# Kernel optimization log

Measured on AMD Instinct MI355X. Metric: run time of the kernel, lower is better.

Reference implementation:

```python
import jax, jax.numpy as jnp
import numpy as np
from jax import lax

# ---- config (mirrors init_kwargs) ----
B, CIN, T, WIDTH = 32, 8, 256, 128
COUT = 64
K = (5, 5)
PAD = (2, 2)            # ceil((k-1)*dilation/2) per dim
OUT_W = 128             # output_shape
EPS = 1e-8
BETA0 = 0.9             # beta 'constant' init, one_per_layer
B0 = 1.0                # b 'constant' init
SIGMA0 = 10.0
MAX_SPK = 3.0           # Max_spikes_per_run


@jax.custom_vjp
def spike_fn(mthr, sigma):
    # Surrogate Heaviside: hard threshold fwd, sigmoid-derivative surrogate bwd.
    return (mthr > 0).astype(mthr.dtype)

def _spike_fwd(mthr, sigma):
    return spike_fn(mthr, sigma), (mthr, sigma)

def _spike_bwd(res, g):
    mthr, sigma = res
    sg = jax.nn.sigmoid(sigma * mthr)
    return (g * sigma * sg * (1.0 - sg), jnp.zeros_like(sigma))

spike_fn.defvjp(_spike_fwd, _spike_bwd)


def setup_inputs() -> dict:
    key = jax.random.key(0)
    kx, kw = jax.random.split(key)
    x = jax.random.normal(kx, (B, CIN, T, WIDTH), dtype=jnp.float32)
    w_std = 1.0 * np.sqrt(1.0 / (CIN * K[0] * K[1]))
    w = jax.random.normal(kw, (COUT, CIN, K[0], K[1]), dtype=jnp.float32) * w_std
    b = jnp.full((COUT,), B0, dtype=jnp.float32)          # clamped >= 0
    beta = jnp.array([BETA0], dtype=jnp.float32)           # one_per_layer, clamped to [0,1]
    sigma = jnp.array([SIGMA0], dtype=jnp.float32)         # surrogate_sigma_mode 'one'
    return {"x": x, "w": w, "b": b, "beta": beta, "sigma": sigma}


def _forward(x, w, b, beta, sigma):
    # conv over (time, width) with 'same'-style padding, then truncate width
    conv_x = lax.conv_general_dilated(
        x, w, window_strides=(1, 1),
        padding=((PAD[0], PAD[0]), (PAD[1], PAD[1])),
        rhs_dilation=(1, 1),
        dimension_numbers=("NCHW", "OIHW", "NCHW"))
    conv_x = conv_x[:, :, :, :OUT_W]                      # [B, COUT, T, OUT_W]

    d = jnp.einsum("oikl,eikl->oe", w, w)                 # lateral matrix [COUT, COUT]
    norm = jnp.sum(w * w, axis=(1, 2, 3))                 # [COUT]
    inv_norm = 1.0 / (norm + EPS)
    beta_s = beta[0]

    conv_seq = jnp.transpose(conv_x, (2, 0, 1, 3))        # [T, B, COUT, OUT_W]

    def step(carry, inp_t):
        mem, spk, prev = carry
        rst = jnp.einsum("bcw,cd->bdw", spk, d)           # lateral reset
        # Leaky neuron, soft reset
        mem = (mem - rst) * beta_s + inp_t * (1.0 - beta_s)
        mthr = mem * inv_norm[None, :, None] - b[None, :, None]
        s = (MAX_SPK - prev) * spike_fn(mthr, sigma)      # spike_limit=True
        prev = prev + s
        return (mem, s, prev), s

    zeros = jnp.zeros((B, COUT, OUT_W), dtype=x.dtype)
    (_, _, _), spk_rec = lax.scan(step, (zeros, zeros, zeros), conv_seq)
    # spk_rec: [T, B, COUT, OUT_W]

    loss = 0.5 * jnp.mean(spk_rec ** 2)                   # 'squared'
    spk_spread = jnp.max(jnp.sum(spk_rec, axis=(1, 2, 3))) / (B * COUT * OUT_W)  # 'max'

    output = jnp.transpose(spk_rec, (1, 2, 0, 3))         # [B, COUT, T, OUT_W]
    return output, loss, spk_spread


def reference(x, w, b, beta, sigma):
    return _forward(x, w, b, beta, sigma)
```

## Files before the change

kernel.cpp:

```cpp
#include <hip/hip_runtime.h>
#include <cstdint>


#define NB 32
#define NC 8
#define NT 256
#define NW 128
#define NO 64
#define WT 16
#define TC 8
#define NROWS 12
#define NCHUNK (NT / TC)
#define XCOLS 20
#define XTILE (NC * NROWS * XCOLS)

__global__ __launch_bounds__(1024)
void prep_kernel(const float* __restrict__ w, float* __restrict__ d3,
                 float* __restrict__ invn, unsigned int* __restrict__ gfires)
{
    __shared__ float wsh[NO * 200];
    const int tid = threadIdx.x;
    for (int i = tid; i < NO * 200; i += 1024) wsh[i] = w[i];
    if (tid < NT) gfires[tid] = 0u;
    __syncthreads();
#pragma unroll
    for (int p = 0; p < 4; ++p) {
        int idx = p * 1024 + tid;
        int o = idx >> 6, e = idx & 63;
        float acc = 0.0f;
        for (int i = 0; i < 200; i += 4) {
            float4 av = *(const float4*)&wsh[o * 200 + i];
            float4 bv = *(const float4*)&wsh[e * 200 + i];
            acc += av.x * bv.x + av.y * bv.y + av.z * bv.z + av.w * bv.w;
        }
        d3[idx] = 3.0f * acc;
        if (o == e) invn[o] = 1.0f / (acc + 1e-8f);
    }
}

__global__ __launch_bounds__(512, 2)
void spk_kernel(const float* __restrict__ x, const float* __restrict__ wglob,
                const float* __restrict__ bias, const float* __restrict__ beta_p,
                const float* __restrict__ d3g, const float* __restrict__ invng,
                float* __restrict__ out, unsigned int* __restrict__ gfires)
{
    __shared__ float wsm[NC * 25 * NO];
    __shared__ float d3s[NO * NO];
    __shared__ float xsh[2][NC][NROWS][XCOLS];
    __shared__ unsigned short tf[2][NO][8];
    __shared__ unsigned int sf[NT];

    const int tid  = threadIdx.x;
    const int lane = tid & 63;
    const int wv   = tid >> 6;
    const int bb   = blockIdx.x >> 3;
    const int w0   = (blockIdx.x & 7) * WT;

    for (int i = tid; i < NC * 25 * NO; i += 512) {
        int co = i & 63; int r = i >> 6;
        int kw = r % 5; int r2 = r / 5; int kt = r2 % 5; int c = r2 / 5;
        wsm[i] = wglob[((co * NC + c) * 5 + kt) * 5 + kw];
    }
    for (int i = tid; i < NO * NO; i += 512) d3s[i] = d3g[i];
    for (int i = tid; i < NT; i += 512) sf[i] = 0u;

    const size_t xbbase = (size_t)bb * NC * NT * NW;
#pragma unroll
    for (int k = 0; k < 4; ++k) {
        int i = tid + k * 512;
        if (i < XTILE) {
            int c = i / (NROWS * XCOLS); int rem = i - c * (NROWS * XCOLS);
            int row = rem / XCOLS; int col = rem - row * XCOLS;
            int tg = row - 2, wg = w0 + col - 2;
            float v = 0.0f;
            if (tg >= 0 && tg < NT && wg >= 0 && wg < NW)
                v = x[xbbase + ((size_t)c * NT + tg) * NW + wg];
            (&xsh[0][0][0][0])[i] = v;
        }
    }

    const float invn = invng[lane];
    const float bco  = bias[lane];
    const float beta = beta_p[0];
    const float omb  = 1.0f - beta;

    float mem0 = 0.f, mem1 = 0.f;
    unsigned int fired = 0u;
    unsigned long long pm0 = 0ull, pm1 = 0ull;

    const int sq = tid & 3;
    const int srow = tid >> 2;

    __syncthreads();

#pragma unroll 1
    for (int ch = 0; ch < NCHUNK; ++ch) {
        const int buf = ch & 1;
        const int tbase = ch * TC;

        float sr0 = 0.f, sr1 = 0.f, sr2 = 0.f, sr3 = 0.f;
        if (ch + 1 < NCHUNK) {
#pragma unroll
            for (int k = 0; k < 4; ++k) {
                int i = tid + k * 512;
                float v = 0.0f;
                if (i < XTILE) {
                    int c = i / (NROWS * XCOLS); int rem = i - c * (NROWS * XCOLS);
                    int row = rem / XCOLS; int col = rem - row * XCOLS;
                    int tg = tbase + 6 + row, wg = w0 + col - 2;
                    if (tg < NT && wg >= 0 && wg < NW)
                        v = x[xbbase + ((size_t)c * NT + tg) * NW + wg];
                }
                if (k == 0) sr0 = v; else if (k == 1) sr1 = v;
                else if (k == 2) sr2 = v; else sr3 = v;
            }
        }

        if (ch > 0) {
            const int pbuf = buf ^ 1;
            const int tprev = tbase - TC;
#pragma unroll
            for (int p = 0; p < 4; ++p) {
                int rowi = p * 128 + srow;
                int co = rowi >> 3, tt = rowi & 7;
                unsigned int codes = *(const unsigned int*)&tf[pbuf][co][sq * 2];
                float4 v;
                v.x = (((codes      ) & 0xffu) == (unsigned)tt) ? 3.0f : 0.0f;
                v.y = (((codes >>  8) & 0xffu) == (unsigned)tt) ? 3.0f : 0.0f;
                v.z = (((codes >> 16) & 0xffu) == (unsigned)tt) ? 3.0f : 0.0f;
                v.w = (((codes >> 24) & 0xffu) == (unsigned)tt) ? 3.0f : 0.0f;
                *(float4*)(out + (((size_t)(bb * NO + co) * NT + tprev + tt) * NW + w0 + sq * 4)) = v;
            }
        }

        float acc[TC][2];
#pragma unroll
        for (int t = 0; t < TC; ++t) { acc[t][0] = 0.f; acc[t][1] = 0.f; }

#pragma unroll 1
        for (int c = 0; c < NC; ++c) {
            float2 xr[NROWS][3];
#pragma unroll
            for (int r = 0; r < NROWS; ++r) {
                const float* base = &xsh[buf][c][r][2 * wv];
                xr[r][0] = *(const float2*)(base);
                xr[r][1] = *(const float2*)(base + 2);
                xr[r][2] = *(const float2*)(base + 4);
            }
#pragma unroll
            for (int kt = 0; kt < 5; ++kt) {
                const float* wp = &wsm[((c * 5 + kt) * 5) * 64 + lane];
                float wk0 = wp[0], wk1 = wp[64], wk2 = wp[128], wk3 = wp[192], wk4 = wp[256];
#pragma unroll
                for (int t = 0; t < TC; ++t) {
                    float2 a = xr[t + kt][0], b2 = xr[t + kt][1], c2 = xr[t + kt][2];
                    acc[t][0] += wk0 * a.x + wk1 * a.y + wk2 * b2.x + wk3 * b2.y + wk4 * c2.x;
                    acc[t][1] += wk0 * a.y + wk1 * b2.x + wk2 * b2.y + wk3 * c2.x + wk4 * c2.y;
                }
            }
        }

        unsigned int tfc0 = 0xffu, tfc1 = 0xffu;
#pragma unroll
        for (int tt = 0; tt < TC; ++tt) {
            float r0 = 0.f, r1 = 0.f;
            if (pm0 | pm1) {
                unsigned long long m = pm0;
                while (m) { int c = __builtin_ctzll(m); m &= m - 1; r0 += d3s[c * 64 + lane]; }
                m = pm1;
                while (m) { int c = __builtin_ctzll(m); m &= m - 1; r1 += d3s[c * 64 + lane]; }
            }
            mem0 = (mem0 - r0) * beta + acc[tt][0] * omb;
            mem1 = (mem1 - r1) * beta + acc[tt][1] * omb;
            bool f0 = !(fired & 1u) && (mem0 * invn - bco > 0.0f);
            bool f1 = !(fired & 2u) && (mem1 * invn - bco > 0.0f);
            pm0 = __ballot(f0);
            pm1 = __ballot(f1);
            if (f0) { fired |= 1u; tfc0 = (unsigned)tt; }
            if (f1) { fired |= 2u; tfc1 = (unsigned)tt; }
            unsigned int cnt = (unsigned)(__popcll(pm0) + __popcll(pm1));
            if (lane == 0 && cnt) atomicAdd(&sf[tbase + tt], cnt);
        }
        tf[buf][lane][wv] = (unsigned short)(tfc0 | (tfc1 << 8));

        if (ch + 1 < NCHUNK) {
            float* dst = &xsh[buf ^ 1][0][0][0];
#pragma unroll
            for (int k = 0; k < 4; ++k) {
                int i = tid + k * 512;
                float v = (k == 0) ? sr0 : (k == 1) ? sr1 : (k == 2) ? sr2 : sr3;
                if (i < XTILE) dst[i] = v;
            }
        }
        __syncthreads();
    }

    {
        const int pbuf = (NCHUNK - 1) & 1;
        const int tprev = NT - TC;
#pragma unroll
        for (int p = 0; p < 4; ++p) {
            int rowi = p * 128 + srow;
            int co = rowi >> 3, tt = rowi & 7;
            unsigned int codes = *(const unsigned int*)&tf[pbuf][co][sq * 2];
            float4 v;
            v.x = (((codes      ) & 0xffu) == (unsigned)tt) ? 3.0f : 0.0f;
            v.y = (((codes >>  8) & 0xffu) == (unsigned)tt) ? 3.0f : 0.0f;
            v.z = (((codes >> 16) & 0xffu) == (unsigned)tt) ? 3.0f : 0.0f;
            v.w = (((codes >> 24) & 0xffu) == (unsigned)tt) ? 3.0f : 0.0f;
            *(float4*)(out + (((size_t)(bb * NO + co) * NT + tprev + tt) * NW + w0 + sq * 4)) = v;
        }
    }

    if (tid < NT) atomicAdd(&gfires[tid], sf[tid]);
}

__global__ __launch_bounds__(256)
void fin_kernel(const unsigned int* __restrict__ gfires, float* __restrict__ out)
{
    const int tid = threadIdx.x;
    unsigned int v = gfires[tid];
    unsigned int s = v, m = v;
    for (int off = 32; off > 0; off >>= 1) {
        s += __shfl_down(s, off);
        unsigned int o = __shfl_down(m, off);
        m = m > o ? m : o;
    }
    __shared__ unsigned int ls[4], lm[4];
    if ((tid & 63) == 0) { ls[tid >> 6] = s; lm[tid >> 6] = m; }
    __syncthreads();
    if (tid == 0) {
        unsigned int ts = 0, tm = 0;
        for (int i = 0; i < 4; ++i) { ts += ls[i]; tm = tm > lm[i] ? tm : lm[i]; }
        out[67108864] = 4.5f * (float)ts / 67108864.0f;
        out[67108865] = 3.0f * (float)tm / 262144.0f;
    }
}

extern "C" void kernel_launch(void* const* d_in, const int* in_sizes, int n_in,
                              void* d_out, int out_size, void* d_ws, size_t ws_size,
                              hipStream_t stream)
{
    const float* x    = (const float*)d_in[0];
    const float* w    = (const float*)d_in[1];
    const float* b    = (const float*)d_in[2];
    const float* beta = (const float*)d_in[3];

    float* out  = (float*)d_out;
    float* wsf  = (float*)d_ws;
    float* d3   = wsf;
    float* invn = wsf + 4096;
    unsigned int* gf = (unsigned int*)(wsf + 4160);

    prep_kernel<<<1, 1024, 0, stream>>>(w, d3, invn, gf);
    spk_kernel<<<256, 512, 0, stream>>>(x, w, b, beta, d3, invn, out, gf);
    fin_kernel<<<1, 256, 0, stream>>>(gf, out);
}
```

Measured before the change: 778.0 us.

## Precompute prefetch/store addresses, unroll channel loop, explicit FMAs, relax launch bounds

Moves the per-chunk index arithmetic for the x prefetch and the spike output stores out of the time-chunk loop into precomputed per-thread pointers and offsets. The channel loop is unrolled by two and the conv accumulation is written as explicit fmaf chains. Launch bounds drop from two blocks per SIMD to one, giving the compiler more registers for the extra live state. The cost is possible occupancy loss, since fewer waves are resident to hide latency in this serial-scan kernel.

```diff
diff --git a/kernel.cpp b/kernel.cpp
--- a/kernel.cpp
+++ b/kernel.cpp
@@ -1,5 +1,6 @@
 #include <hip/hip_runtime.h>
 #include <cstdint>
+#include <math.h>
 
 
 #define NB 32
@@ -38,7 +39,7 @@
     }
 }
 
-__global__ __launch_bounds__(512, 2)
+__global__ __launch_bounds__(512, 1)
 void spk_kernel(const float* __restrict__ x, const float* __restrict__ wglob,
                 const float* __restrict__ bias, const float* __restrict__ beta_p,
                 const float* __restrict__ d3g, const float* __restrict__ invng,
@@ -65,6 +66,38 @@
     for (int i = tid; i < NT; i += 512) sf[i] = 0u;
 
     const size_t xbbase = (size_t)bb * NC * NT * NW;
+
+    const float* pf_ptr[4];
+    int  pf_idx[4];
+    int  pf_row[4];
+    bool pf_okw[4];
+#pragma unroll
+    for (int k = 0; k < 4; ++k) {
+        int i = tid + k * 512;
+        if (i < XTILE) {
+            int c = i / (NROWS * XCOLS); int rem = i - c * (NROWS * XCOLS);
+            int row = rem / XCOLS; int col = rem - row * XCOLS;
+            int wg = w0 + col - 2;
+            pf_idx[k] = i; pf_row[k] = row;
+            pf_okw[k] = (wg >= 0 && wg < NW);
+            pf_ptr[k] = x + xbbase + ((size_t)c * NT + 6 + row) * NW + (wg < 0 ? 0 : wg);
+        } else { pf_idx[k] = -1; pf_row[k] = 0; pf_okw[k] = false; pf_ptr[k] = x; }
+    }
+
+    const int sq = tid & 3;
+    const int srow = tid >> 2;
+    int    sp_tfidx[4];
+    int    sp_tt[4];
+    float* sp_out[4];
+#pragma unroll
+    for (int p = 0; p < 4; ++p) {
+        int rowi = p * 128 + srow;
+        int co = rowi >> 3, tt = rowi & 7;
+        sp_tfidx[p] = co * 8 + sq * 2;
+        sp_tt[p] = tt;
+        sp_out[p] = out + (((size_t)(bb * NO + co) * NT + tt) * NW + w0 + sq * 4);
+    }
+
 #pragma unroll
     for (int k = 0; k < 4; ++k) {
         int i = tid + k * 512;
@@ -88,9 +121,6 @@
     unsigned int fired = 0u;
     unsigned long long pm0 = 0ull, pm1 = 0ull;
 
-    const int sq = tid & 3;
-    const int srow = tid >> 2;
-
     __syncthreads();
 
 #pragma unroll 1
@@ -98,38 +128,31 @@
         const int buf = ch & 1;
         const int tbase = ch * TC;
 
-        float sr0 = 0.f, sr1 = 0.f, sr2 = 0.f, sr3 = 0.f;
+        float sr[4];
         if (ch + 1 < NCHUNK) {
 #pragma unroll
             for (int k = 0; k < 4; ++k) {
-                int i = tid + k * 512;
                 float v = 0.0f;
-                if (i < XTILE) {
-                    int c = i / (NROWS * XCOLS); int rem = i - c * (NROWS * XCOLS);
-                    int row = rem / XCOLS; int col = rem - row * XCOLS;
-                    int tg = tbase + 6 + row, wg = w0 + col - 2;
-                    if (tg < NT && wg >= 0 && wg < NW)
-                        v = x[xbbase + ((size_t)c * NT + tg) * NW + wg];
-                }
-                if (k == 0) sr0 = v; else if (k == 1) sr1 = v;
-                else if (k == 2) sr2 = v; else sr3 = v;
+                int tg = (ch << 3) + 6 + pf_row[k];
+                if (pf_okw[k] && tg < NT)
+                    v = pf_ptr[k][(size_t)ch * (TC * NW)];
+                sr[k] = v;
             }
         }
 
         if (ch > 0) {
-            const int pbuf = buf ^ 1;
-            const int tprev = tbase - TC;
+            const unsigned short* tfp = &tf[buf ^ 1][0][0];
+            const size_t oadv = (size_t)(ch - 1) * (TC * NW);
 #pragma unroll
             for (int p = 0; p < 4; ++p) {
-                int rowi = p * 128 + srow;
-                int co = rowi >> 3, tt = rowi & 7;
-                unsigned int codes = *(const unsigned int*)&tf[pbuf][co][sq * 2];
+                unsigned int codes = *(const unsigned int*)(tfp + sp_tfidx[p]);
+                unsigned int tt = (unsigned)sp_tt[p];
                 float4 v;
-                v.x = (((codes      ) & 0xffu) == (unsigned)tt) ? 3.0f : 0.0f;
-                v.y = (((codes >>  8) & 0xffu) == (unsigned)tt) ? 3.0f : 0.0f;
-                v.z = (((codes >> 16) & 0xffu) == (unsigned)tt) ? 3.0f : 0.0f;
-                v.w = (((codes >> 24) & 0xffu) == (unsigned)tt) ? 3.0f : 0.0f;
-                *(float4*)(out + (((size_t)(bb * NO + co) * NT + tprev + tt) * NW + w0 + sq * 4)) = v;
+                v.x = (((codes      ) & 0xffu) == tt) ? 3.0f : 0.0f;
+                v.y = (((codes >>  8) & 0xffu) == tt) ? 3.0f : 0.0f;
+                v.z = (((codes >> 16) & 0xffu) == tt) ? 3.0f : 0.0f;
+                v.w = (((codes >> 24) & 0xffu) == tt) ? 3.0f : 0.0f;
+                *(float4*)(sp_out[p] + oadv) = v;
             }
         }
 
@@ -137,7 +160,7 @@
 #pragma unroll
         for (int t = 0; t < TC; ++t) { acc[t][0] = 0.f; acc[t][1] = 0.f; }
 
-#pragma unroll 1
+#pragma unroll 2
         for (int c = 0; c < NC; ++c) {
             float2 xr[NROWS][3];
 #pragma unroll
@@ -154,8 +177,18 @@
 #pragma unroll
                 for (int t = 0; t < TC; ++t) {
                     float2 a = xr[t + kt][0], b2 = xr[t + kt][1], c2 = xr[t + kt][2];
-                    acc[t][0] += wk0 * a.x + wk1 * a.y + wk2 * b2.x + wk3 * b2.y + wk4 * c2.x;
-                    acc[t][1] += wk0 * a.y + wk1 * b2.x + wk2 * b2.y + wk3 * c2.x + wk4 * c2.y;
+                    float u0 = acc[t][0], u1 = acc[t][1];
+                    u0 = fmaf(wk0, a.x,  u0);
+                    u0 = fmaf(wk1, a.y,  u0);
+                    u0 = fmaf(wk2, b2.x, u0);
+                    u0 = fmaf(wk3, b2.y, u0);
+                    u0 = fmaf(wk4, c2.x, u0);
+                    u1 = fmaf(wk0, a.y,  u1);
+                    u1 = fmaf(wk1, b2.x, u1);
+                    u1 = fmaf(wk2, b2.y, u1);
+                    u1 = fmaf(wk3, c2.x, u1);
+                    u1 = fmaf(wk4, c2.y, u1);
+                    acc[t][0] = u0; acc[t][1] = u1;
                 }
             }
         }
@@ -187,28 +220,25 @@
             float* dst = &xsh[buf ^ 1][0][0][0];
 #pragma unroll
             for (int k = 0; k < 4; ++k) {
-                int i = tid + k * 512;
-                float v = (k == 0) ? sr0 : (k == 1) ? sr1 : (k == 2) ? sr2 : sr3;
-                if (i < XTILE) dst[i] = v;
+                if (pf_idx[k] >= 0) dst[pf_idx[k]] = sr[k];
             }
         }
         __syncthreads();
     }
 
     {
-        const int pbuf = (NCHUNK - 1) & 1;
-        const int tprev = NT - TC;
+        const unsigned short* tfp = &tf[(NCHUNK - 1) & 1][0][0];
+        const size_t oadv = (size_t)(NCHUNK - 1) * (TC * NW);
 #pragma unroll
         for (int p = 0; p < 4; ++p) {
-            int rowi = p * 128 + srow;
-            int co = rowi >> 3, tt = rowi & 7;
-            unsigned int codes = *(const unsigned int*)&tf[pbuf][co][sq * 2];
+            unsigned int codes = *(const unsigned int*)(tfp + sp_tfidx[p]);
+            unsigned int tt = (unsigned)sp_tt[p];
             float4 v;
-            v.x = (((codes      ) & 0xffu) == (unsigned)tt) ? 3.0f : 0.0f;
-            v.y = (((codes >>  8) & 0xffu) == (unsigned)tt) ? 3.0f : 0.0f;
-            v.z = (((codes >> 16) & 0xffu) == (unsigned)tt) ? 3.0f : 0.0f;
-            v.w = (((codes >> 24) & 0xffu) == (unsigned)tt) ? 3.0f : 0.0f;
-            *(float4*)(out + (((size_t)(bb * NO + co) * NT + tprev + tt) * NW + w0 + sq * 4)) = v;
+            v.x = (((codes      ) & 0xffu) == tt) ? 3.0f : 0.0f;
+            v.y = (((codes >>  8) & 0xffu) == tt) ? 3.0f : 0.0f;
+            v.z = (((codes >> 16) & 0xffu) == tt) ? 3.0f : 0.0f;
+            v.w = (((codes >> 24) & 0xffu) == tt) ? 3.0f : 0.0f;
+            *(float4*)(sp_out[p] + oadv) = v;
         }
     }
 
```

Result: faster. 752.8 us (-3.2%).
